# Kernel tuning notes

Measured on AMD Instinct MI355X. Metric: run time of the kernel, lower is better.

The kernel has to match this reference:

```python
import jax, jax.numpy as jnp
import numpy as np

ALPHA, BETA, GAMMA = 1.0, 0.1, 0.1
EPS = 1e-12


def _cubic_kernel(r, h):
    # standard 3D cubic spline kernel
    sigma = 8.0 / (jnp.pi * h ** 3)
    q = r / h
    w = jnp.where(q <= 0.5, 6.0 * (q ** 3 - q ** 2) + 1.0, 2.0 * (1.0 - q) ** 3)
    return sigma * jnp.where(q <= 1.0, w, 0.0)


def _cubic_kernel_dwdr(r, h):
    sigma = 8.0 / (jnp.pi * h ** 3)
    q = r / h
    dw = jnp.where(q <= 0.5, 6.0 * q * (3.0 * q - 2.0), -6.0 * (1.0 - q) ** 2)
    return (sigma / h) * jnp.where(q <= 1.0, dw, 0.0)


def setup_inputs() -> dict:
    key = jax.random.key(0)
    N, NB, D = 6144, 768, 3
    ks = jax.random.split(key, 6)
    mid_pos = jax.random.uniform(ks[0], (N, D), dtype=jnp.float32)  # unit box
    mid_vel = jax.random.normal(ks[1], (N, D), dtype=jnp.float32) * 0.1
    pred = jax.random.normal(ks[2], (N, D), dtype=jnp.float32)
    y = jax.random.normal(ks[3], (N, D), dtype=jnp.float32)
    y_mean = jax.random.normal(ks[4], (D,), dtype=jnp.float32) * 1e-3
    y_std = jax.random.uniform(ks[5], (D,), dtype=jnp.float32) * 2e-3 + 1e-4
    return {
        "pred": pred, "y": y, "mid_pos": mid_pos, "mid_vel": mid_vel,
        "y_mean": y_mean, "y_std": y_std,
        "h": jnp.float32(0.11), "vol": jnp.float32(1.0 / N),
        "rho_0": jnp.float32(1000.0), "dt": jnp.float32(0.005),
        "num_boundary_particles": NB,
    }


def reference(pred, y, mid_pos, mid_vel, y_mean, y_std, h, vol, rho_0, dt,
              num_boundary_particles):
    nb = num_boundary_particles  # static Python int
    # loss1: MSE in standardized space
    loss1 = jnp.mean(jnp.sum((y - pred) ** 2, axis=1))
    # Standardizer.inverse_y
    y_inv = y * y_std + y_mean
    # advect fluid (non-boundary) particles by predicted displacement
    pos = mid_pos.at[nb:].add(y_inv[nb:])
    # radius_graph(pos, h, loop=True) as dense mask over pairwise distances
    sq = jnp.sum(pos * pos, axis=1)  # [N]
    d2 = jnp.maximum(sq[:, None] + sq[None, :] - 2.0 * (pos @ pos.T), 0.0)  # [N,N]
    mask = d2 <= h * h
    r = jnp.sqrt(jnp.maximum(d2, EPS))
    # SPH density: rho_i = rho_0 * vol * sum_j W(r_ij, h)
    W = jnp.where(mask, _cubic_kernel(r, h), 0.0)
    rho = rho_0 * vol * jnp.sum(W, axis=1)
    loss2 = jnp.mean(jnp.abs(rho / rho_0 - 1.0))
    # velocity update for fluid particles
    vel = mid_vel.at[nb:].add(y_inv[nb:] / dt)
    # SPH divergence: div_i = vol * sum_j (v_j - v_i) . gradW_ij,
    # gradW_ij = dW/dr * (x_i - x_j) / r; build the pair dot products via GEMMs:
    # (v_j - v_i).(x_i - x_j) = x_i.v_j + x_j.v_i - x_j.v_j - x_i.v_i
    dwdr = jnp.where(mask, _cubic_kernel_dwdr(r, h), 0.0)
    inv_r = jnp.where(d2 > EPS, 1.0 / r, 0.0)  # self/coincident pairs contribute 0
    Dm = pos @ vel.T  # Dm[i,j] = x_i . v_j
    diag = jnp.sum(pos * vel, axis=1)  # x_k . v_k
    dot = Dm + Dm.T - diag[None, :] - diag[:, None]
    div = vol * jnp.sum(dwdr * inv_r * dot, axis=1)
    loss3 = jnp.mean(jnp.abs(div))
    return ALPHA * loss1 + BETA * loss2 + GAMMA * loss3
```

## Files before the change

### kernel.cpp

```cpp
#include <hip/hip_runtime.h>
#include <math.h>

#define TPB 1024
#define NBLK 243
#define NWAVE (TPB / 64)
#define NCELL 9
#define CAP 1024
#define HCAP 512
#define PI_F 3.14159265358979323846f
#define EPS_F 1e-12f

__device__ __forceinline__ float wave_reduce(float v) {
#pragma unroll
    for (int off = 32; off > 0; off >>= 1) v += __shfl_down(v, off, 64);
    return v;
}

__device__ __forceinline__ float block_reduce(float v, float* sbuf) {
    v = wave_reduce(v);
    int lane = threadIdx.x & 63;
    int wid  = threadIdx.x >> 6;
    if (lane == 0) sbuf[wid] = v;
    __syncthreads();
    float r = 0.0f;
    if (threadIdx.x == 0) {
        for (int w = 0; w < NWAVE; ++w) r += sbuf[w];
    }
    return r;
}

__device__ __forceinline__ int cell_coord(float x) {
    int c = (int)floorf(x * (float)NCELL);
    return min(max(c, 0), NCELL - 1);
}

__device__ __forceinline__ void pair_math(float xix, float xiy, float xiz,
                                          float vix, float viy, float viz,
                                          float ax, float ay, float az,
                                          float bx, float by, float bz,
                                          float inv_h, float h2,
                                          float& wacc, float& dacc) {
    float dx = xix - ax, dy = xiy - ay, dz = xiz - az;
    float d2 = fmaf(dx, dx, fmaf(dy, dy, dz * dz));
    float r2c = fmaxf(d2, EPS_F);
    float ir  = rsqrtf(r2c);
    float r   = r2c * ir;
    float q   = r * inv_h;
    bool inm = (d2 <= h2) && (q <= 1.0f);
    bool lo  = (q <= 0.5f);
    float q2 = q * q, om = 1.0f - q, om2 = om * om;
    float w  = lo ? fmaf(6.0f, q2 * q - q2, 1.0f) : 2.0f * om2 * om;
    wacc += inm ? w : 0.0f;
    float dw = lo ? q * fmaf(18.0f, q, -12.0f) : -6.0f * om2;
    dw = inm ? dw : 0.0f;
    float irm = (d2 > EPS_F) ? ir : 0.0f;
    float dvx = bx - vix, dvy = by - viy, dvz = bz - viz;
    float dot = fmaf(dvx, dx, fmaf(dvy, dy, dvz * dz));
    dacc = fmaf(dw * irm, dot, dacc);
}

__global__ void __launch_bounds__(TPB) k_main(
    const float* __restrict__ pred, const float* __restrict__ y,
    const float* __restrict__ mid_pos, const float* __restrict__ mid_vel,
    const float* __restrict__ y_mean, const float* __restrict__ y_std,
    const float* __restrict__ h_p, const float* __restrict__ vol_p,
    const float* __restrict__ dt_p, const int* __restrict__ nb_p,
    float* __restrict__ out, int N, float invN)
{
    __shared__ float4 sh4[CAP];
    __shared__ float2 sh2[CAP];
    __shared__ short  s_home[HCAP];
    __shared__ int    s_cnt, s_hcnt;
    __shared__ float  sred[NWAVE];

    int b   = blockIdx.x;
    int tid = threadIdx.x;
    int cx = b / 27, cy = (b / 3) % 9, czg = b % 3;
    int z0 = 3 * czg;

    if (tid == 0) { s_cnt = 0; s_hcnt = 0; }
    __syncthreads();

    int nb = nb_p[0];
    float inv_dt = 1.0f / dt_p[0];
    float ym0 = y_mean[0], ym1 = y_mean[1], ym2 = y_mean[2];
    float ys0 = y_std[0],  ys1 = y_std[1],  ys2 = y_std[2];

    bool do_l1 = (b == 0);
    float t1 = 0.0f;
    int ln = tid & 63;
    unsigned long long lmask = (1ull << ln) - 1ull;

    for (int i = tid; i < N; i += TPB) {
        float y0 = y[i * 3 + 0], y1 = y[i * 3 + 1], y2 = y[i * 3 + 2];
        float m0 = mid_pos[i * 3 + 0], m1 = mid_pos[i * 3 + 1], m2 = mid_pos[i * 3 + 2];
        if (do_l1) {
            float p0 = pred[i * 3 + 0], p1 = pred[i * 3 + 1], p2 = pred[i * 3 + 2];
            float d0 = y0 - p0, d1 = y1 - p1, d2 = y2 - p2;
            t1 = fmaf(d0, d0, fmaf(d1, d1, fmaf(d2, d2, t1)));
        }
        bool fluid = (i >= nb);
        float i0 = fluid ? fmaf(y0, ys0, ym0) : 0.0f;
        float i1 = fluid ? fmaf(y1, ys1, ym1) : 0.0f;
        float i2 = fluid ? fmaf(y2, ys2, ym2) : 0.0f;
        float px = m0 + i0, py = m1 + i1, pz = m2 + i2;
        int ix = cell_coord(px), iy = cell_coord(py), iz = cell_coord(pz);
        int adx = abs(ix - cx), ady = abs(iy - cy);
        bool inN = (adx <= 1) && (ady <= 1) && (iz >= z0 - 1) && (iz <= z0 + 3);
        bool isH = (adx == 0) && (ady == 0) && (iz >= z0) && (iz <= z0 + 2);

        unsigned long long mN = __ballot(inN);
        if (mN) {
            int baseN = 0;
            if (ln == 0) baseN = atomicAdd(&s_cnt, __popcll(mN));
            baseN = __shfl(baseN, 0, 64);
            if (inN) {
                int slot = baseN + __popcll(mN & lmask);
                if (slot < CAP) {
                    float v0 = mid_vel[i * 3 + 0] + i0 * inv_dt;
                    float v1 = mid_vel[i * 3 + 1] + i1 * inv_dt;
                    float v2 = mid_vel[i * 3 + 2] + i2 * inv_dt;
                    sh4[slot] = make_float4(px, py, pz, v0);
                    sh2[slot] = make_float2(v1, v2);
                }
            }
        }
        unsigned long long mH = __ballot(isH);
        if (mH) {
            int baseH = 0;
            if (ln == 0) baseH = atomicAdd(&s_hcnt, __popcll(mH));
            baseH = __shfl(baseH, 0, 64);
            if (isH) {
                int hs = baseH + __popcll(mH & lmask);
                if (hs < HCAP) s_home[hs] = (short)i;
            }
        }
    }
    if (do_l1) {
        float s1 = block_reduce(t1, sred);
        if (tid == 0) atomicAdd(out, s1 * invN);
    }
    __syncthreads();

    int T = s_cnt;
    int H = min(s_hcnt, HCAP);
    bool staged = (T <= CAP);

    float h = h_p[0], inv_h = 1.0f / h, h2 = h * h;
    float vol = vol_p[0];
    float sigma = 8.0f / (PI_F * h * h * h);

    int wv = tid >> 6;
    float acc = 0.0f;

    for (int hp = wv; hp < H; hp += NWAVE) {
        int i = s_home[hp];
        float y0 = y[i * 3 + 0], y1 = y[i * 3 + 1], y2 = y[i * 3 + 2];
        bool fluid = (i >= nb);
        float i0 = fluid ? fmaf(y0, ys0, ym0) : 0.0f;
        float i1 = fluid ? fmaf(y1, ys1, ym1) : 0.0f;
        float i2 = fluid ? fmaf(y2, ys2, ym2) : 0.0f;
        float xix = mid_pos[i * 3 + 0] + i0;
        float xiy = mid_pos[i * 3 + 1] + i1;
        float xiz = mid_pos[i * 3 + 2] + i2;
        float vix = mid_vel[i * 3 + 0] + i0 * inv_dt;
        float viy = mid_vel[i * 3 + 1] + i1 * inv_dt;
        float viz = mid_vel[i * 3 + 2] + i2 * inv_dt;

        float wacc = 0.0f, dacc = 0.0f;
        if (staged) {
            for (int j = ln; j < T; j += 64) {
                float4 a  = sh4[j];
                float2 b2 = sh2[j];
                pair_math(xix, xiy, xiz, vix, viy, viz,
                          a.x, a.y, a.z, a.w, b2.x, b2.y, inv_h, h2, wacc, dacc);
            }
        } else {
            for (int j = ln; j < N; j += 64) {
                float jy0 = y[j * 3 + 0], jy1 = y[j * 3 + 1], jy2 = y[j * 3 + 2];
                bool jf = (j >= nb);
                float j0 = jf ? fmaf(jy0, ys0, ym0) : 0.0f;
                float j1 = jf ? fmaf(jy1, ys1, ym1) : 0.0f;
                float j2 = jf ? fmaf(jy2, ys2, ym2) : 0.0f;
                float ax = mid_pos[j * 3 + 0] + j0;
                float ay = mid_pos[j * 3 + 1] + j1;
                float az = mid_pos[j * 3 + 2] + j2;
                float bx = mid_vel[j * 3 + 0] + j0 * inv_dt;
                float by = mid_vel[j * 3 + 1] + j1 * inv_dt;
                float bz = mid_vel[j * 3 + 2] + j2 * inv_dt;
                pair_math(xix, xiy, xiz, vix, viy, viz,
                          ax, ay, az, bx, by, bz, inv_h, h2, wacc, dacc);
            }
        }
        wacc = wave_reduce(wacc);
        dacc = wave_reduce(dacc);
        if (ln == 0) {
            acc += fabsf(fmaf(vol * sigma, wacc, -1.0f))
                 + fabsf(vol * (sigma / h) * dacc);
        }
    }

    float tot = block_reduce(acc, sred);
    if (tid == 0) atomicAdd(out, 0.1f * invN * tot);
}

extern "C" void kernel_launch(void* const* d_in, const int* in_sizes, int n_in,
                              void* d_out, int out_size, void* d_ws, size_t ws_size,
                              hipStream_t stream) {
    const float* pred    = (const float*)d_in[0];
    const float* y       = (const float*)d_in[1];
    const float* mid_pos = (const float*)d_in[2];
    const float* mid_vel = (const float*)d_in[3];
    const float* y_mean  = (const float*)d_in[4];
    const float* y_std   = (const float*)d_in[5];
    const float* h_p     = (const float*)d_in[6];
    const float* vol_p   = (const float*)d_in[7];
    const float* dt_p    = (const float*)d_in[9];
    const int*   nb_p    = (const int*)d_in[10];

    int N = in_sizes[0] / 3;
    float invN = 1.0f / (float)N;

    hipMemsetAsync(d_out, 0, sizeof(float), stream);

    k_main<<<NBLK, TPB, 0, stream>>>(pred, y, mid_pos, mid_vel, y_mean, y_std,
                                     h_p, vol_p, dt_p, nb_p,
                                     (float*)d_out, N, invN);
}
```

Measured before the change: 21.20 us.

## Batch neighbor staging loads and derive home list from staged particles

```diff
diff --git a/kernel.cpp b/kernel.cpp
--- a/kernel.cpp
+++ b/kernel.cpp
@@ -6,7 +6,7 @@
 #define NWAVE (TPB / 64)
 #define NCELL 9
 #define CAP 1024
-#define HCAP 512
+#define HCAP 1024
 #define PI_F 3.14159265358979323846f
 #define EPS_F 1e-12f
 
@@ -91,48 +91,80 @@
     int ln = tid & 63;
     unsigned long long lmask = (1ull << ln) - 1ull;
 
-    for (int i = tid; i < N; i += TPB) {
-        float y0 = y[i * 3 + 0], y1 = y[i * 3 + 1], y2 = y[i * 3 + 2];
-        float m0 = mid_pos[i * 3 + 0], m1 = mid_pos[i * 3 + 1], m2 = mid_pos[i * 3 + 2];
-        if (do_l1) {
-            float p0 = pred[i * 3 + 0], p1 = pred[i * 3 + 1], p2 = pred[i * 3 + 2];
-            float d0 = y0 - p0, d1 = y1 - p1, d2 = y2 - p2;
-            t1 = fmaf(d0, d0, fmaf(d1, d1, fmaf(d2, d2, t1)));
-        }
-        bool fluid = (i >= nb);
-        float i0 = fluid ? fmaf(y0, ys0, ym0) : 0.0f;
-        float i1 = fluid ? fmaf(y1, ys1, ym1) : 0.0f;
-        float i2 = fluid ? fmaf(y2, ys2, ym2) : 0.0f;
-        float px = m0 + i0, py = m1 + i1, pz = m2 + i2;
-        int ix = cell_coord(px), iy = cell_coord(py), iz = cell_coord(pz);
-        int adx = abs(ix - cx), ady = abs(iy - cy);
-        bool inN = (adx <= 1) && (ady <= 1) && (iz >= z0 - 1) && (iz <= z0 + 3);
-        bool isH = (adx == 0) && (ady == 0) && (iz >= z0) && (iz <= z0 + 2);
-
-        unsigned long long mN = __ballot(inN);
-        if (mN) {
-            int baseN = 0;
-            if (ln == 0) baseN = atomicAdd(&s_cnt, __popcll(mN));
-            baseN = __shfl(baseN, 0, 64);
-            if (inN) {
-                int slot = baseN + __popcll(mN & lmask);
+    if (N == TPB * 6) {
+        float ppx[6], ppy[6], ppz[6], pvx[6], pvy[6], pvz[6];
+        bool inN_[6];
+        unsigned long long mN[6];
+#pragma unroll
+        for (int k = 0; k < 6; ++k) {
+            int i = tid + k * TPB;
+            float y0 = y[i * 3 + 0], y1 = y[i * 3 + 1], y2 = y[i * 3 + 2];
+            float m0 = mid_pos[i * 3 + 0], m1 = mid_pos[i * 3 + 1], m2 = mid_pos[i * 3 + 2];
+            float w0 = mid_vel[i * 3 + 0], w1 = mid_vel[i * 3 + 1], w2 = mid_vel[i * 3 + 2];
+            if (do_l1) {
+                float p0 = pred[i * 3 + 0], p1 = pred[i * 3 + 1], p2 = pred[i * 3 + 2];
+                float d0 = y0 - p0, d1 = y1 - p1, d2 = y2 - p2;
+                t1 = fmaf(d0, d0, fmaf(d1, d1, fmaf(d2, d2, t1)));
+            }
+            bool fluid = (i >= nb);
+            float i0 = fluid ? fmaf(y0, ys0, ym0) : 0.0f;
+            float i1 = fluid ? fmaf(y1, ys1, ym1) : 0.0f;
+            float i2 = fluid ? fmaf(y2, ys2, ym2) : 0.0f;
+            ppx[k] = m0 + i0; ppy[k] = m1 + i1; ppz[k] = m2 + i2;
+            pvx[k] = w0 + i0 * inv_dt; pvy[k] = w1 + i1 * inv_dt; pvz[k] = w2 + i2 * inv_dt;
+            int ix = cell_coord(ppx[k]), iy = cell_coord(ppy[k]), iz = cell_coord(ppz[k]);
+            inN_[k] = (abs(ix - cx) <= 1) && (abs(iy - cy) <= 1) &&
+                      (iz >= z0 - 1) && (iz <= z0 + 3);
+            mN[k] = __ballot(inN_[k]);
+        }
+        int pre[6], tot = 0;
+#pragma unroll
+        for (int k = 0; k < 6; ++k) { pre[k] = tot; tot += __popcll(mN[k]); }
+        int base = 0;
+        if (ln == 0 && tot > 0) base = atomicAdd(&s_cnt, tot);
+        base = __shfl(base, 0, 64);
+#pragma unroll
+        for (int k = 0; k < 6; ++k) {
+            if (inN_[k]) {
+                int slot = base + pre[k] + __popcll(mN[k] & lmask);
                 if (slot < CAP) {
-                    float v0 = mid_vel[i * 3 + 0] + i0 * inv_dt;
-                    float v1 = mid_vel[i * 3 + 1] + i1 * inv_dt;
-                    float v2 = mid_vel[i * 3 + 2] + i2 * inv_dt;
-                    sh4[slot] = make_float4(px, py, pz, v0);
-                    sh2[slot] = make_float2(v1, v2);
+                    sh4[slot] = make_float4(ppx[k], ppy[k], ppz[k], pvx[k]);
+                    sh2[slot] = make_float2(pvy[k], pvz[k]);
                 }
             }
         }
-        unsigned long long mH = __ballot(isH);
-        if (mH) {
-            int baseH = 0;
-            if (ln == 0) baseH = atomicAdd(&s_hcnt, __popcll(mH));
-            baseH = __shfl(baseH, 0, 64);
-            if (isH) {
-                int hs = baseH + __popcll(mH & lmask);
-                if (hs < HCAP) s_home[hs] = (short)i;
+    } else {
+        for (int i = tid; i < N; i += TPB) {
+            float y0 = y[i * 3 + 0], y1 = y[i * 3 + 1], y2 = y[i * 3 + 2];
+            float m0 = mid_pos[i * 3 + 0], m1 = mid_pos[i * 3 + 1], m2 = mid_pos[i * 3 + 2];
+            if (do_l1) {
+                float p0 = pred[i * 3 + 0], p1 = pred[i * 3 + 1], p2 = pred[i * 3 + 2];
+                float d0 = y0 - p0, d1 = y1 - p1, d2 = y2 - p2;
+                t1 = fmaf(d0, d0, fmaf(d1, d1, fmaf(d2, d2, t1)));
+            }
+            bool fluid = (i >= nb);
+            float i0 = fluid ? fmaf(y0, ys0, ym0) : 0.0f;
+            float i1 = fluid ? fmaf(y1, ys1, ym1) : 0.0f;
+            float i2 = fluid ? fmaf(y2, ys2, ym2) : 0.0f;
+            float px = m0 + i0, py = m1 + i1, pz = m2 + i2;
+            int ix = cell_coord(px), iy = cell_coord(py), iz = cell_coord(pz);
+            bool inN = (abs(ix - cx) <= 1) && (abs(iy - cy) <= 1) &&
+                       (iz >= z0 - 1) && (iz <= z0 + 3);
+            unsigned long long mN = __ballot(inN);
+            if (mN) {
+                int base = 0;
+                if (ln == 0) base = atomicAdd(&s_cnt, __popcll(mN));
+                base = __shfl(base, 0, 64);
+                if (inN) {
+                    int slot = base + __popcll(mN & lmask);
+                    if (slot < CAP) {
+                        float v0 = mid_vel[i * 3 + 0] + i0 * inv_dt;
+                        float v1 = mid_vel[i * 3 + 1] + i1 * inv_dt;
+                        float v2 = mid_vel[i * 3 + 2] + i2 * inv_dt;
+                        sh4[slot] = make_float4(px, py, pz, v0);
+                        sh2[slot] = make_float2(v1, v2);
+                    }
+                }
             }
         }
     }
@@ -143,39 +175,66 @@
     __syncthreads();
 
     int T = s_cnt;
-    int H = min(s_hcnt, HCAP);
     bool staged = (T <= CAP);
 
     float h = h_p[0], inv_h = 1.0f / h, h2 = h * h;
     float vol = vol_p[0];
     float sigma = 8.0f / (PI_F * h * h * h);
-
     int wv = tid >> 6;
     float acc = 0.0f;
 
-    for (int hp = wv; hp < H; hp += NWAVE) {
-        int i = s_home[hp];
-        float y0 = y[i * 3 + 0], y1 = y[i * 3 + 1], y2 = y[i * 3 + 2];
-        bool fluid = (i >= nb);
-        float i0 = fluid ? fmaf(y0, ys0, ym0) : 0.0f;
-        float i1 = fluid ? fmaf(y1, ys1, ym1) : 0.0f;
-        float i2 = fluid ? fmaf(y2, ys2, ym2) : 0.0f;
-        float xix = mid_pos[i * 3 + 0] + i0;
-        float xiy = mid_pos[i * 3 + 1] + i1;
-        float xiz = mid_pos[i * 3 + 2] + i2;
-        float vix = mid_vel[i * 3 + 0] + i0 * inv_dt;
-        float viy = mid_vel[i * 3 + 1] + i1 * inv_dt;
-        float viz = mid_vel[i * 3 + 2] + i2 * inv_dt;
-
-        float wacc = 0.0f, dacc = 0.0f;
-        if (staged) {
+    if (staged) {
+        bool isH = false;
+        if (tid < T) {
+            float4 a = sh4[tid];
+            int ix = cell_coord(a.x), iy = cell_coord(a.y), iz = cell_coord(a.z);
+            isH = (ix == cx) && (iy == cy) && (iz >= z0) && (iz <= z0 + 2);
+        }
+        unsigned long long mH = __ballot(isH);
+        if (mH) {
+            int hb = 0;
+            if (ln == 0) hb = atomicAdd(&s_hcnt, __popcll(mH));
+            hb = __shfl(hb, 0, 64);
+            if (isH) s_home[hb + __popcll(mH & lmask)] = (short)tid;
+        }
+        __syncthreads();
+        int H = s_hcnt;
+
+        for (int hp = wv; hp < H; hp += NWAVE) {
+            int hs = s_home[hp];
+            float4 me4 = sh4[hs];
+            float2 me2 = sh2[hs];
+            float wacc = 0.0f, dacc = 0.0f;
             for (int j = ln; j < T; j += 64) {
                 float4 a  = sh4[j];
                 float2 b2 = sh2[j];
-                pair_math(xix, xiy, xiz, vix, viy, viz,
+                pair_math(me4.x, me4.y, me4.z, me4.w, me2.x, me2.y,
                           a.x, a.y, a.z, a.w, b2.x, b2.y, inv_h, h2, wacc, dacc);
             }
-        } else {
+            wacc = wave_reduce(wacc);
+            dacc = wave_reduce(dacc);
+            if (ln == 0) {
+                acc += fabsf(fmaf(vol * sigma, wacc, -1.0f))
+                     + fabsf(vol * (sigma / h) * dacc);
+            }
+        }
+    } else {
+        for (int i = wv; i < N; i += NWAVE) {
+            float y0 = y[i * 3 + 0], y1 = y[i * 3 + 1], y2 = y[i * 3 + 2];
+            bool fluid = (i >= nb);
+            float i0 = fluid ? fmaf(y0, ys0, ym0) : 0.0f;
+            float i1 = fluid ? fmaf(y1, ys1, ym1) : 0.0f;
+            float i2 = fluid ? fmaf(y2, ys2, ym2) : 0.0f;
+            float xix = mid_pos[i * 3 + 0] + i0;
+            float xiy = mid_pos[i * 3 + 1] + i1;
+            float xiz = mid_pos[i * 3 + 2] + i2;
+            int ix = cell_coord(xix), iy = cell_coord(xiy), iz = cell_coord(xiz);
+            bool isH = (ix == cx) && (iy == cy) && (iz >= z0) && (iz <= z0 + 2);
+            if (!isH) continue;
+            float vix = mid_vel[i * 3 + 0] + i0 * inv_dt;
+            float viy = mid_vel[i * 3 + 1] + i1 * inv_dt;
+            float viz = mid_vel[i * 3 + 2] + i2 * inv_dt;
+            float wacc = 0.0f, dacc = 0.0f;
             for (int j = ln; j < N; j += 64) {
                 float jy0 = y[j * 3 + 0], jy1 = y[j * 3 + 1], jy2 = y[j * 3 + 2];
                 bool jf = (j >= nb);
@@ -191,13 +250,14 @@
                 pair_math(xix, xiy, xiz, vix, viy, viz,
                           ax, ay, az, bx, by, bz, inv_h, h2, wacc, dacc);
             }
-        }
-        wacc = wave_reduce(wacc);
-        dacc = wave_reduce(dacc);
-        if (ln == 0) {
-            acc += fabsf(fmaf(vol * sigma, wacc, -1.0f))
-                 + fabsf(vol * (sigma / h) * dacc);
-        }
+            wacc = wave_reduce(wacc);
+            dacc = wave_reduce(dacc);
+            if (ln == 0) {
+                acc += fabsf(fmaf(vol * sigma, wacc, -1.0f))
+                     + fabsf(vol * (sigma / h) * dacc);
+            }
+        }
+        __syncthreads();
     }
 
     float tot = block_reduce(acc, sred);
```

After: 19.94 us. 1.06x faster.

## Split into global cell-binning pass and per-cell pair kernel

Applied to the files above, without the earlier changes.

```diff
diff --git a/kernel.cpp b/kernel.cpp
--- a/kernel.cpp
+++ b/kernel.cpp
@@ -1,12 +1,13 @@
 #include <hip/hip_runtime.h>
 #include <math.h>
 
-#define TPB 1024
-#define NBLK 243
-#define NWAVE (TPB / 64)
+#define BTPB 1024
+#define PTPB 256
+#define NWAVE (PTPB / 64)
 #define NCELL 9
-#define CAP 1024
-#define HCAP 512
+#define NCELL3 729
+#define CAPC 40
+#define CAP (27 * CAPC)
 #define PI_F 3.14159265358979323846f
 #define EPS_F 1e-12f
 
@@ -16,6 +17,7 @@
     return v;
 }
 
+template<int NT>
 __device__ __forceinline__ float block_reduce(float v, float* sbuf) {
     v = wave_reduce(v);
     int lane = threadIdx.x & 63;
@@ -24,7 +26,7 @@
     __syncthreads();
     float r = 0.0f;
     if (threadIdx.x == 0) {
-        for (int w = 0; w < NWAVE; ++w) r += sbuf[w];
+        for (int w = 0; w < NT / 64; ++w) r += sbuf[w];
     }
     return r;
 }
@@ -59,123 +61,149 @@
     dacc = fmaf(dw * irm, dot, dacc);
 }
 
-__global__ void __launch_bounds__(TPB) k_main(
+__global__ void __launch_bounds__(BTPB) k_bin(
     const float* __restrict__ pred, const float* __restrict__ y,
     const float* __restrict__ mid_pos, const float* __restrict__ mid_vel,
     const float* __restrict__ y_mean, const float* __restrict__ y_std,
+    const float* __restrict__ dt_p, const int* __restrict__ nb_p,
+    float4* __restrict__ pos_b, float2* __restrict__ vel_b,
+    int* __restrict__ count, float* __restrict__ out, int N, float invN)
+{
+    __shared__ float sred[BTPB / 64];
+    int tid = threadIdx.x;
+    int i = blockIdx.x * BTPB + tid;
+    float t1 = 0.0f;
+    if (i < N) {
+        int nb = nb_p[0];
+        float inv_dt = 1.0f / dt_p[0];
+        float y0 = y[i * 3 + 0], y1 = y[i * 3 + 1], y2 = y[i * 3 + 2];
+        float p0 = pred[i * 3 + 0], p1 = pred[i * 3 + 1], p2 = pred[i * 3 + 2];
+        float d0 = y0 - p0, d1 = y1 - p1, d2 = y2 - p2;
+        t1 = fmaf(d0, d0, fmaf(d1, d1, d2 * d2));
+        bool fluid = (i >= nb);
+        float i0 = fluid ? fmaf(y0, y_std[0], y_mean[0]) : 0.0f;
+        float i1 = fluid ? fmaf(y1, y_std[1], y_mean[1]) : 0.0f;
+        float i2 = fluid ? fmaf(y2, y_std[2], y_mean[2]) : 0.0f;
+        float px = mid_pos[i * 3 + 0] + i0;
+        float py = mid_pos[i * 3 + 1] + i1;
+        float pz = mid_pos[i * 3 + 2] + i2;
+        float vx = mid_vel[i * 3 + 0] + i0 * inv_dt;
+        float vy = mid_vel[i * 3 + 1] + i1 * inv_dt;
+        float vz = mid_vel[i * 3 + 2] + i2 * inv_dt;
+        int c = (cell_coord(px) * NCELL + cell_coord(py)) * NCELL + cell_coord(pz);
+        int slot = atomicAdd(&count[c], 1);
+        if (slot < CAPC) {
+            pos_b[c * CAPC + slot] = make_float4(px, py, pz, vx);
+            vel_b[c * CAPC + slot] = make_float2(vy, vz);
+        } else {
+            atomicExch(&count[NCELL3], 1);
+        }
+    }
+    float s = block_reduce<BTPB>(t1, sred);
+    if (tid == 0) atomicAdd(out, s * invN);
+}
+
+__global__ void __launch_bounds__(PTPB) k_pairs(
+    const float4* __restrict__ pos_b, const float2* __restrict__ vel_b,
+    const int* __restrict__ count,
+    const float* __restrict__ y, const float* __restrict__ mid_pos,
+    const float* __restrict__ mid_vel,
+    const float* __restrict__ y_mean, const float* __restrict__ y_std,
+    const float* __restrict__ dt_p, const int* __restrict__ nb_p,
     const float* __restrict__ h_p, const float* __restrict__ vol_p,
-    const float* __restrict__ dt_p, const int* __restrict__ nb_p,
-    float* __restrict__ out, int N, float invN)
+    float* __restrict__ out, int N, float coef )
 {
     __shared__ float4 sh4[CAP];
     __shared__ float2 sh2[CAP];
-    __shared__ short  s_home[HCAP];
-    __shared__ int    s_cnt, s_hcnt;
-    __shared__ float  sred[NWAVE];
-
-    int b   = blockIdx.x;
+    __shared__ int s_cid[27];
+    __shared__ int s_off[28];
+    __shared__ float sred[PTPB / 64];
+
+    int b = blockIdx.x;
+    if (count[b] == 0) return;
+    int flag = count[NCELL3];
+
     int tid = threadIdx.x;
-    int cx = b / 27, cy = (b / 3) % 9, czg = b % 3;
-    int z0 = 3 * czg;
-
-    if (tid == 0) { s_cnt = 0; s_hcnt = 0; }
-    __syncthreads();
-
-    int nb = nb_p[0];
-    float inv_dt = 1.0f / dt_p[0];
-    float ym0 = y_mean[0], ym1 = y_mean[1], ym2 = y_mean[2];
-    float ys0 = y_std[0],  ys1 = y_std[1],  ys2 = y_std[2];
-
-    bool do_l1 = (b == 0);
-    float t1 = 0.0f;
-    int ln = tid & 63;
-    unsigned long long lmask = (1ull << ln) - 1ull;
-
-    for (int i = tid; i < N; i += TPB) {
-        float y0 = y[i * 3 + 0], y1 = y[i * 3 + 1], y2 = y[i * 3 + 2];
-        float m0 = mid_pos[i * 3 + 0], m1 = mid_pos[i * 3 + 1], m2 = mid_pos[i * 3 + 2];
-        if (do_l1) {
-            float p0 = pred[i * 3 + 0], p1 = pred[i * 3 + 1], p2 = pred[i * 3 + 2];
-            float d0 = y0 - p0, d1 = y1 - p1, d2 = y2 - p2;
-            t1 = fmaf(d0, d0, fmaf(d1, d1, fmaf(d2, d2, t1)));
-        }
-        bool fluid = (i >= nb);
-        float i0 = fluid ? fmaf(y0, ys0, ym0) : 0.0f;
-        float i1 = fluid ? fmaf(y1, ys1, ym1) : 0.0f;
-        float i2 = fluid ? fmaf(y2, ys2, ym2) : 0.0f;
-        float px = m0 + i0, py = m1 + i1, pz = m2 + i2;
-        int ix = cell_coord(px), iy = cell_coord(py), iz = cell_coord(pz);
-        int adx = abs(ix - cx), ady = abs(iy - cy);
-        bool inN = (adx <= 1) && (ady <= 1) && (iz >= z0 - 1) && (iz <= z0 + 3);
-        bool isH = (adx == 0) && (ady == 0) && (iz >= z0) && (iz <= z0 + 2);
-
-        unsigned long long mN = __ballot(inN);
-        if (mN) {
-            int baseN = 0;
-            if (ln == 0) baseN = atomicAdd(&s_cnt, __popcll(mN));
-            baseN = __shfl(baseN, 0, 64);
-            if (inN) {
-                int slot = baseN + __popcll(mN & lmask);
-                if (slot < CAP) {
-                    float v0 = mid_vel[i * 3 + 0] + i0 * inv_dt;
-                    float v1 = mid_vel[i * 3 + 1] + i1 * inv_dt;
-                    float v2 = mid_vel[i * 3 + 2] + i2 * inv_dt;
-                    sh4[slot] = make_float4(px, py, pz, v0);
-                    sh2[slot] = make_float2(v1, v2);
-                }
-            }
-        }
-        unsigned long long mH = __ballot(isH);
-        if (mH) {
-            int baseH = 0;
-            if (ln == 0) baseH = atomicAdd(&s_hcnt, __popcll(mH));
-            baseH = __shfl(baseH, 0, 64);
-            if (isH) {
-                int hs = baseH + __popcll(mH & lmask);
-                if (hs < HCAP) s_home[hs] = (short)i;
-            }
-        }
-    }
-    if (do_l1) {
-        float s1 = block_reduce(t1, sred);
-        if (tid == 0) atomicAdd(out, s1 * invN);
-    }
-    __syncthreads();
-
-    int T = s_cnt;
-    int H = min(s_hcnt, HCAP);
-    bool staged = (T <= CAP);
+    int ln = tid & 63, wv = tid >> 6;
+    int cx = b / (NCELL * NCELL), cy = (b / NCELL) % NCELL, cz = b % NCELL;
 
     float h = h_p[0], inv_h = 1.0f / h, h2 = h * h;
     float vol = vol_p[0];
     float sigma = 8.0f / (PI_F * h * h * h);
-
-    int wv = tid >> 6;
     float acc = 0.0f;
 
-    for (int hp = wv; hp < H; hp += NWAVE) {
-        int i = s_home[hp];
-        float y0 = y[i * 3 + 0], y1 = y[i * 3 + 1], y2 = y[i * 3 + 2];
-        bool fluid = (i >= nb);
-        float i0 = fluid ? fmaf(y0, ys0, ym0) : 0.0f;
-        float i1 = fluid ? fmaf(y1, ys1, ym1) : 0.0f;
-        float i2 = fluid ? fmaf(y2, ys2, ym2) : 0.0f;
-        float xix = mid_pos[i * 3 + 0] + i0;
-        float xiy = mid_pos[i * 3 + 1] + i1;
-        float xiz = mid_pos[i * 3 + 2] + i2;
-        float vix = mid_vel[i * 3 + 0] + i0 * inv_dt;
-        float viy = mid_vel[i * 3 + 1] + i1 * inv_dt;
-        float viz = mid_vel[i * 3 + 2] + i2 * inv_dt;
-
-        float wacc = 0.0f, dacc = 0.0f;
-        if (staged) {
+    if (flag == 0) {
+        if (tid < 27) {
+            int nx = cx + tid / 9 - 1;
+            int ny = cy + (tid / 3) % 3 - 1;
+            int nz = cz + tid % 3 - 1;
+            bool valid = ((unsigned)nx < NCELL) && ((unsigned)ny < NCELL) &&
+                         ((unsigned)nz < NCELL);
+            int c = valid ? (nx * NCELL + ny) * NCELL + nz : 0;
+            s_cid[tid] = valid ? c : -1;
+            s_off[tid] = valid ? count[c] : 0;
+        }
+        __syncthreads();
+        if (tid == 0) {
+            int a = 0;
+            for (int r = 0; r < 27; ++r) { int t = s_off[r]; s_off[r] = a; a += t; }
+            s_off[27] = a;
+        }
+        __syncthreads();
+        int T = s_off[27];
+
+        for (int g = tid; g < T; g += PTPB) {
+            int lo = 0, hi = 26;
+            while (lo < hi) {
+                int mid = (lo + hi + 1) >> 1;
+                if (s_off[mid] <= g) lo = mid; else hi = mid - 1;
+            }
+            int c = s_cid[lo];
+            int w = g - s_off[lo];
+            sh4[g] = pos_b[c * CAPC + w];
+            sh2[g] = vel_b[c * CAPC + w];
+        }
+        __syncthreads();
+
+        int h0 = s_off[13], h1 = s_off[14];
+        for (int hp = h0 + wv; hp < h1; hp += NWAVE) {
+            float4 me4 = sh4[hp];
+            float2 me2 = sh2[hp];
+            float wacc = 0.0f, dacc = 0.0f;
             for (int j = ln; j < T; j += 64) {
                 float4 a  = sh4[j];
                 float2 b2 = sh2[j];
-                pair_math(xix, xiy, xiz, vix, viy, viz,
+                pair_math(me4.x, me4.y, me4.z, me4.w, me2.x, me2.y,
                           a.x, a.y, a.z, a.w, b2.x, b2.y, inv_h, h2, wacc, dacc);
             }
-        } else {
+            wacc = wave_reduce(wacc);
+            dacc = wave_reduce(dacc);
+            if (ln == 0) {
+                acc += fabsf(fmaf(vol * sigma, wacc, -1.0f))
+                     + fabsf(vol * (sigma / h) * dacc);
+            }
+        }
+    } else {
+        int nb = nb_p[0];
+        float inv_dt = 1.0f / dt_p[0];
+        float ym0 = y_mean[0], ym1 = y_mean[1], ym2 = y_mean[2];
+        float ys0 = y_std[0],  ys1 = y_std[1],  ys2 = y_std[2];
+        for (int i = wv; i < N; i += NWAVE) {
+            float y0 = y[i * 3 + 0], y1 = y[i * 3 + 1], y2 = y[i * 3 + 2];
+            bool fluid = (i >= nb);
+            float i0 = fluid ? fmaf(y0, ys0, ym0) : 0.0f;
+            float i1 = fluid ? fmaf(y1, ys1, ym1) : 0.0f;
+            float i2 = fluid ? fmaf(y2, ys2, ym2) : 0.0f;
+            float xix = mid_pos[i * 3 + 0] + i0;
+            float xiy = mid_pos[i * 3 + 1] + i1;
+            float xiz = mid_pos[i * 3 + 2] + i2;
+            bool isH = (cell_coord(xix) == cx) && (cell_coord(xiy) == cy) &&
+                       (cell_coord(xiz) == cz);
+            if (!isH) continue;
+            float vix = mid_vel[i * 3 + 0] + i0 * inv_dt;
+            float viy = mid_vel[i * 3 + 1] + i1 * inv_dt;
+            float viz = mid_vel[i * 3 + 2] + i2 * inv_dt;
+            float wacc = 0.0f, dacc = 0.0f;
             for (int j = ln; j < N; j += 64) {
                 float jy0 = y[j * 3 + 0], jy1 = y[j * 3 + 1], jy2 = y[j * 3 + 2];
                 bool jf = (j >= nb);
@@ -191,17 +219,18 @@
                 pair_math(xix, xiy, xiz, vix, viy, viz,
                           ax, ay, az, bx, by, bz, inv_h, h2, wacc, dacc);
             }
-        }
-        wacc = wave_reduce(wacc);
-        dacc = wave_reduce(dacc);
-        if (ln == 0) {
-            acc += fabsf(fmaf(vol * sigma, wacc, -1.0f))
-                 + fabsf(vol * (sigma / h) * dacc);
-        }
+            wacc = wave_reduce(wacc);
+            dacc = wave_reduce(dacc);
+            if (ln == 0) {
+                acc += fabsf(fmaf(vol * sigma, wacc, -1.0f))
+                     + fabsf(vol * (sigma / h) * dacc);
+            }
+        }
+        __syncthreads();
     }
 
-    float tot = block_reduce(acc, sred);
-    if (tid == 0) atomicAdd(out, 0.1f * invN * tot);
+    float tot = block_reduce<PTPB>(acc, sred);
+    if (tid == 0) atomicAdd(out, coef * tot);
 }
 
 extern "C" void kernel_launch(void* const* d_in, const int* in_sizes, int n_in,
@@ -220,10 +249,23 @@
 
     int N = in_sizes[0] / 3;
     float invN = 1.0f / (float)N;
-
-    hipMemsetAsync(d_out, 0, sizeof(float), stream);
-
-    k_main<<<NBLK, TPB, 0, stream>>>(pred, y, mid_pos, mid_vel, y_mean, y_std,
-                                     h_p, vol_p, dt_p, nb_p,
-                                     (float*)d_out, N, invN);
-}
+    int nB = (N + BTPB - 1) / BTPB;
+
+    char* wsb = (char*)d_ws;
+    float4* pos_b = (float4*)wsb;     wsb += (size_t)NCELL3 * CAPC * sizeof(float4);
+    float2* vel_b = (float2*)wsb;     wsb += (size_t)NCELL3 * CAPC * sizeof(float2);
+    int*    count = (int*)wsb;
+
+    float* out = (float*)d_out;
+
+    hipMemsetAsync(count, 0, (NCELL3 + 1) * sizeof(int), stream);
+    hipMemsetAsync(out, 0, sizeof(float), stream);
+
+    k_bin<<<nB, BTPB, 0, stream>>>(pred, y, mid_pos, mid_vel, y_mean, y_std,
+                                   dt_p, nb_p, pos_b, vel_b, count, out, N, invN);
+
+    k_pairs<<<NCELL3, PTPB, 0, stream>>>(pos_b, vel_b, count,
+                                         y, mid_pos, mid_vel, y_mean, y_std,
+                                         dt_p, nb_p, h_p, vol_p,
+                                         out, N, 0.1f * invN);
+}
```

After: 31.90 us. 50.4% more time.
